# Optimization experiments

Measured on AMD Instinct MI355X. Metric: run time of the kernel, lower is better.

Reference implementation:

```python
import jax, jax.numpy as jnp
import numpy as np

EPS = 1e-5
P, B, T, C = 2, 8, 1024, 1024
H = 4 * C

def layernorm(x, g, b):
    mu = jnp.mean(x, axis=-1, keepdims=True)
    var = jnp.var(x, axis=-1, keepdims=True)
    return (x - mu) * jax.lax.rsqrt(var + EPS) * g + b

def time_shift(x):
    # ZeroPad2d((0,0,1,-1)): xx[t] = x[t-1], xx[0] = 0 along the T axis
    pad = [(0, 0)] * (x.ndim - 2) + [(1, 0), (0, 0)]
    return jnp.pad(x, pad)[..., :-1, :]

def wkv(time_decay, time_first, k, v):
    # Faithful port of the RWKV-v4 CUDA WKV scan (numerically stable form).
    # k, v: [N, T, C]; time_decay/time_first: [C]
    w = -jnp.exp(time_decay)  # decay (negative)
    u = time_first
    kT = jnp.moveaxis(k, 1, 0)  # [T, N, C]
    vT = jnp.moveaxis(v, 1, 0)
    N = k.shape[0]
    Cc = k.shape[2]

    def step(carry, kv):
        aa, bb, pp = carry
        kk, vv = kv
        ww = u + kk
        p = jnp.maximum(pp, ww)
        e1 = jnp.exp(pp - p)
        e2 = jnp.exp(ww - p)
        y = (e1 * aa + e2 * vv) / (e1 * bb + e2)
        ww2 = w + pp
        p2 = jnp.maximum(ww2, kk)
        e1b = jnp.exp(ww2 - p2)
        e2b = jnp.exp(kk - p2)
        return (e1b * aa + e2b * vv, e1b * bb + e2b, p2), y

    init = (jnp.zeros((N, Cc), jnp.float32), jnp.zeros((N, Cc), jnp.float32),
            jnp.full((N, Cc), -1e38, jnp.float32))
    _, yT = jax.lax.scan(step, init, (kT, vT))
    return jnp.moveaxis(yT, 0, 1)  # [N, T, C]


def setup_inputs() -> dict:
    key = jax.random.key(0)
    ks = jax.random.split(key, 20)
    f32 = jnp.float32
    layer_id, n_layer = 1, 12
    ratio_0_to_1 = layer_id / (n_layer - 1)
    ratio_1_to_almost0 = 1.0 - layer_id / n_layer
    xcurve = (np.arange(C, dtype=np.float32) / C).reshape(1, 1, C)
    decay_speed = -5 + 8 * (np.arange(C, dtype=np.float32) / (C - 1)) ** (0.7 + 1.3 * ratio_0_to_1)
    zigzag = (np.array([(i + 1) % 3 - 1 for i in range(C)], dtype=np.float32)) * 0.5
    time_first = np.ones(C, dtype=np.float32) * np.log(0.3) + zigzag
    mk = np.stack([xcurve ** ratio_1_to_almost0 for _ in range(P)], 0)  # [P,1,1,C]
    mv = np.stack([xcurve ** ratio_1_to_almost0 + 0.3 * ratio_0_to_1 for _ in range(P)], 0)
    mr = np.stack([xcurve ** (0.5 * ratio_1_to_almost0) for _ in range(P)], 0)
    s = 0.02
    return {
        'x': jax.random.normal(ks[0], (P, B, T, C), f32),
        'ln1_g': jnp.ones((C,), f32), 'ln1_b': jnp.zeros((C,), f32),
        'ln2_g': jnp.ones((C,), f32), 'ln2_b': jnp.zeros((C,), f32),
        'time_decay': jnp.asarray(decay_speed, f32),
        'time_first': jnp.asarray(time_first, f32),
        'att_mix_k': jnp.asarray(mk, f32), 'att_mix_v': jnp.asarray(mv, f32),
        'att_mix_r': jnp.asarray(mr, f32),
        'Wk': jax.random.normal(ks[1], (C, C), f32) * s,
        'Wv': jax.random.normal(ks[2], (C, C), f32) * s,
        'Wr': jax.random.normal(ks[3], (C, C), f32) * s,
        'Wo': jax.random.normal(ks[4], (C, C), f32) * s,
        'cm_mix_k': jnp.asarray(mk, f32), 'cm_mix_r': jnp.asarray(mk, f32),
        'Wck': jax.random.normal(ks[5], (H, C), f32) * s,
        'Wcr': jax.random.normal(ks[6], (C, C), f32) * s,
        'Wcv': jax.random.normal(ks[7], (C, H), f32) * s,
    }


def reference(x, ln1_g, ln1_b, ln2_g, ln2_b, time_decay, time_first,
              att_mix_k, att_mix_v, att_mix_r, Wk, Wv, Wr, Wo,
              cm_mix_k, cm_mix_r, Wck, Wcr, Wcv):
    p, b, t, c = x.shape
    # --- TimeMix branch: x = x + Wo @ (sigmoid(r) * WKV(k, v)) ---
    h = layernorm(x, ln1_g, ln1_b)
    xx = time_shift(h)
    xk = h * att_mix_k + xx * (1 - att_mix_k)
    xv = h * att_mix_v + xx * (1 - att_mix_v)
    xr = h * att_mix_r + xx * (1 - att_mix_r)
    k = jnp.einsum('pbtc,dc->pbtd', xk, Wk)
    v = jnp.einsum('pbtc,dc->pbtd', xv, Wv)
    sr = jax.nn.sigmoid(jnp.einsum('pbtc,dc->pbtd', xr, Wr))
    y = wkv(time_decay, time_first,
            k.reshape(p * b, t, c), v.reshape(p * b, t, c)).reshape(p, b, t, c)
    x = x + jnp.einsum('pbtc,dc->pbtd', sr * y, Wo)
    # --- ChannelMix branch ---
    h = layernorm(x, ln2_g, ln2_b)
    xx = time_shift(h)
    xk = h * cm_mix_k + xx * (1 - cm_mix_k)
    xr = h * cm_mix_r + xx * (1 - cm_mix_r)
    kk = jnp.einsum('pbtc,hc->pbth', xk, Wck)
    kk = jnp.square(jax.nn.relu(kk))
    kv = jnp.einsum('pbth,ch->pbtc', kk, Wcv)
    out = jax.nn.sigmoid(jnp.einsum('pbtc,dc->pbtd', xr, Wcr)) * kv
    return x + out
```

## Files before the change

kernel.cpp:

```cpp
#include <hip/hip_runtime.h>

#define T_SEQ 1024
#define C_DIM 1024
#define H_DIM 4096
#define M_ROWS 16384
#define CHUNKS 16
#define CLEN 64

typedef _Float16 f16x8 __attribute__((ext_vector_type(8)));
typedef _Float16 f16x4 __attribute__((ext_vector_type(4)));
typedef float    f32x4 __attribute__((ext_vector_type(4)));

#define AS1 __attribute__((address_space(1)))
#define AS3 __attribute__((address_space(3)))

__device__ __forceinline__ void gload_lds16(const void* g, void* l) {
  __builtin_amdgcn_global_load_lds((const AS1 void*)g, (AS3 void*)l, 16, 0, 0);
}

__device__ __forceinline__ float sigmoidf_(float x) {
  return 1.0f / (1.0f + __expf(-x));
}

struct CvtArgs {
  const float* src[7];
  _Float16*    dst[7];
  int n4[7];
  int start[8];
};

__global__ __launch_bounds__(256) void cvt_all_kernel(CvtArgs a) {
  const int bid = blockIdx.x;
  int s = 0;
#pragma unroll
  for (int j = 0; j < 7; ++j) s += (bid >= a.start[j + 1]) ? 1 : 0;
  const int i = (bid - a.start[s]) * 256 + threadIdx.x;
  if (i >= a.n4[s]) return;
  f32x4 v = reinterpret_cast<const f32x4*>(a.src[s])[i];
  f16x4 o;
  o[0] = (_Float16)v[0]; o[1] = (_Float16)v[1];
  o[2] = (_Float16)v[2]; o[3] = (_Float16)v[3];
  reinterpret_cast<f16x4*>(a.dst[s])[i] = o;
}

__global__ __launch_bounds__(256) void ln_kernel(const float* __restrict__ x,
    const float* __restrict__ g, const float* __restrict__ b,
    _Float16* __restrict__ h) {
  const int row  = blockIdx.x * 4 + (threadIdx.x >> 6);
  const int lane = threadIdx.x & 63;
  const f32x4* xr = reinterpret_cast<const f32x4*>(x + (size_t)row * C_DIM);
  f32x4 v[4];
  float s = 0.f, sq = 0.f;
#pragma unroll
  for (int i = 0; i < 4; ++i) {
    v[i] = xr[i * 64 + lane];
#pragma unroll
    for (int j = 0; j < 4; ++j) { s += v[i][j]; sq += v[i][j] * v[i][j]; }
  }
#pragma unroll
  for (int off = 32; off > 0; off >>= 1) {
    s  += __shfl_xor(s, off, 64);
    sq += __shfl_xor(sq, off, 64);
  }
  const float mu   = s * (1.0f / C_DIM);
  const float var  = sq * (1.0f / C_DIM) - mu * mu;
  const float rstd = rsqrtf(var + 1e-5f);
  const f32x4* g4 = reinterpret_cast<const f32x4*>(g);
  const f32x4* b4 = reinterpret_cast<const f32x4*>(b);
  f16x4* h4 = reinterpret_cast<f16x4*>(h + (size_t)row * C_DIM);
#pragma unroll
  for (int i = 0; i < 4; ++i) {
    f32x4 gg = g4[i * 64 + lane];
    f32x4 bb = b4[i * 64 + lane];
    f16x4 o;
#pragma unroll
    for (int j = 0; j < 4; ++j)
      o[j] = (_Float16)((v[i][j] - mu) * rstd * gg[j] + bb[j]);
    h4[i * 64 + lane] = o;
  }
}

__global__ __launch_bounds__(256) void mix3_kernel(const _Float16* __restrict__ h,
    const float* __restrict__ mk, const float* __restrict__ mv, const float* __restrict__ mr,
    _Float16* __restrict__ xk, _Float16* __restrict__ xv, _Float16* __restrict__ xr) {
  const int i  = blockIdx.x * 256 + threadIdx.x;
  const int m  = i >> 7;
  const int c0 = (i & 127) << 3;
  const int p  = m >> 13;
  const int t  = m & (T_SEQ - 1);
  const f16x8* h8 = reinterpret_cast<const f16x8*>(h);
  f16x8 hc = h8[i];
  f16x8 hp;
#pragma unroll
  for (int j = 0; j < 8; ++j) hp[j] = (_Float16)0.f;
  if (t) hp = h8[i - 128];
  f16x8 ok, ov, orr;
#pragma unroll
  for (int j = 0; j < 8; ++j) {
    const float hcf = (float)hc[j], hpf = (float)hp[j];
    const float a = mk[p * C_DIM + c0 + j];
    const float c = mv[p * C_DIM + c0 + j];
    const float d = mr[p * C_DIM + c0 + j];
    ok[j]  = (_Float16)(hcf * a + hpf * (1.f - a));
    ov[j]  = (_Float16)(hcf * c + hpf * (1.f - c));
    orr[j] = (_Float16)(hcf * d + hpf * (1.f - d));
  }
  reinterpret_cast<f16x8*>(xk)[i] = ok;
  reinterpret_cast<f16x8*>(xv)[i] = ov;
  reinterpret_cast<f16x8*>(xr)[i] = orr;
}

__global__ __launch_bounds__(256) void mix2_kernel(const _Float16* __restrict__ h,
    const float* __restrict__ mk, const float* __restrict__ mr,
    _Float16* __restrict__ xk, _Float16* __restrict__ xr) {
  const int i  = blockIdx.x * 256 + threadIdx.x;
  const int m  = i >> 7;
  const int c0 = (i & 127) << 3;
  const int p  = m >> 13;
  const int t  = m & (T_SEQ - 1);
  const f16x8* h8 = reinterpret_cast<const f16x8*>(h);
  f16x8 hc = h8[i];
  f16x8 hp;
#pragma unroll
  for (int j = 0; j < 8; ++j) hp[j] = (_Float16)0.f;
  if (t) hp = h8[i - 128];
  f16x8 ok, orr;
#pragma unroll
  for (int j = 0; j < 8; ++j) {
    const float hcf = (float)hc[j], hpf = (float)hp[j];
    const float a = mk[p * C_DIM + c0 + j];
    const float d = mr[p * C_DIM + c0 + j];
    ok[j]  = (_Float16)(hcf * a + hpf * (1.f - a));
    orr[j] = (_Float16)(hcf * d + hpf * (1.f - d));
  }
  reinterpret_cast<f16x8*>(xk)[i] = ok;
  reinterpret_cast<f16x8*>(xr)[i] = orr;
}

__global__ __launch_bounds__(1024, 1) void wkv_kernel(const _Float16* __restrict__ k,
    const _Float16* __restrict__ v, const _Float16* __restrict__ r,
    const float* __restrict__ td, const float* __restrict__ tf,
    _Float16* __restrict__ a_out) {
  __shared__ float sA[CHUNKS][64];
  __shared__ float sB[CHUNKS][64];
  __shared__ float sP[CHUNKS][64];
  const int tid   = threadIdx.x;
  const int chunk = tid >> 6;
  const int ch    = tid & 63;
  const int n     = blockIdx.x >> 4;
  const int cg    = blockIdx.x & 15;
  const int c     = cg * 64 + ch;
  const float w = -__expf(td[c]);
  const float u = tf[c];
  const size_t cbase = (size_t)n * T_SEQ * C_DIM + (size_t)chunk * CLEN * C_DIM + c;

  float aa = 0.f, bb = 0.f, pp = -1e38f;
  for (int s = 0; s < CLEN; ++s) {
    const size_t idx = cbase + (size_t)s * C_DIM;
    const float kk = (float)k[idx];
    const float vv = (float)v[idx];
    const float ww2 = w + pp;
    const float p2  = fmaxf(ww2, kk);
    const float e1b = __expf(ww2 - p2);
    const float e2b = __expf(kk - p2);
    aa = e1b * aa + e2b * vv;
    bb = e1b * bb + e2b;
    pp = p2;
  }
  sA[chunk][ch] = aa; sB[chunk][ch] = bb; sP[chunk][ch] = pp;
  __syncthreads();

  if (chunk == 0) {
    float pa = 0.f, pb = 0.f, ppr = -1e38f;
    const float wL = w * (float)CLEN;
    for (int j = 0; j < CHUNKS; ++j) {
      const float la = sA[j][ch], lb = sB[j][ch], lp = sP[j][ch];
      sA[j][ch] = pa; sB[j][ch] = pb; sP[j][ch] = ppr;
      const float dp = wL + ppr;
      const float np = fmaxf(dp, lp);
      const float e1 = __expf(dp - np);
      const float e2 = __expf(lp - np);
      pa  = e1 * pa + e2 * la;
      pb  = e1 * pb + e2 * lb;
      ppr = np;
    }
  }
  __syncthreads();

  aa = sA[chunk][ch]; bb = sB[chunk][ch]; pp = sP[chunk][ch];
  for (int s = 0; s < CLEN; ++s) {
    const size_t idx = cbase + (size_t)s * C_DIM;
    const float kk = (float)k[idx];
    const float vv = (float)v[idx];
    const float ww = u + kk;
    const float p  = fmaxf(pp, ww);
    const float e1 = __expf(pp - p);
    const float e2 = __expf(ww - p);
    const float yv = __fdividef(e1 * aa + e2 * vv, e1 * bb + e2);
    const float sr = sigmoidf_((float)r[idx]);
    a_out[idx] = (_Float16)(sr * yv);
    const float ww2 = w + pp;
    const float p2  = fmaxf(ww2, kk);
    const float e1b = __expf(ww2 - p2);
    const float e2b = __expf(kk - p2);
    aa = e1b * aa + e2b * vv;
    bb = e1b * bb + e2b;
    pp = p2;
  }
}

#define GBAR() do { __builtin_amdgcn_sched_barrier(0); \
                    __builtin_amdgcn_s_barrier(); \
                    __builtin_amdgcn_sched_barrier(0); } while (0)
#define WVN(n) do { asm volatile("s_waitcnt vmcnt(" #n ")" ::: "memory"); \
                    __builtin_amdgcn_sched_barrier(0); } while (0)
#define WLN(n) do { asm volatile("s_waitcnt lgkmcnt(" #n ")" ::: "memory"); \
                    __builtin_amdgcn_sched_barrier(0); } while (0)
#define SCHED() __builtin_amdgcn_sched_barrier(0)
#define STAGE(op, SRC, row0, k0, bb) do { \
    _Pragma("unroll") \
    for (int c_ = 0; c_ < 2; ++c_) { \
      gload_lds16((SRC) + (size_t)((row0) + c_ * 64) * K + (k0), \
                  &lds[bb][op][((size_t)((row0) + c_ * 64) << 6) + dbase]); \
    } } while (0)
#define RD_A4(dst, mh, kk_) do { \
    _Pragma("unroll") for (int i_ = 0; i_ < 4; ++i_) \
      dst[i_][kk_] = *reinterpret_cast<const f16x8*>( \
        &lds[bi][0][((wr * 128 + (mh) * 64 + i_ * 16 + frow) << 6) + \
                    ((((kk_) << 5) + fk) ^ fxorh)]); \
  } while (0)
#define RD_B4(kk_) do { \
    _Pragma("unroll") for (int j_ = 0; j_ < 4; ++j_) \
      bf[j_][kk_] = *reinterpret_cast<const f16x8*>( \
        &lds[bi][1][((wcn * 64 + j_ * 16 + frow) << 6) + \
                    ((((kk_) << 5) + fk) ^ fxorh)]); \
  } while (0)
#define MMC(asrc, kk_, half) do { \
    __builtin_amdgcn_s_setprio(1); \
    _Pragma("unroll") for (int i_ = 0; i_ < 4; ++i_) \
    _Pragma("unroll") for (int j_ = 0; j_ < 4; ++j_) \
      acc[(half) * 4 + i_][j_] = __builtin_amdgcn_mfma_f32_16x16x32_f16( \
        asrc[i_][kk_], bf[j_][kk_], acc[(half) * 4 + i_][j_], 0, 0, 0); \
    __builtin_amdgcn_s_setprio(0); \
  } while (0)

template<int EPI>
__global__ __launch_bounds__(512, 2) void gemm_nt_256(
    const _Float16* __restrict__ A, const _Float16* __restrict__ B,
    void* __restrict__ Cv, const float* __restrict__ X,
    const _Float16* __restrict__ KV, int M, int N, int K,
    size_t strideA, size_t strideB, size_t strideCbytes) {
  __shared__ _Float16 lds[2][2][256 * 64];
  const int tid  = threadIdx.x;
  const int wave = tid >> 6;
  const int lane = tid & 63;
  const int wr   = wave >> 2;
  const int wcn  = wave & 3;

  A  = A + (size_t)blockIdx.z * strideA;
  B  = B + (size_t)blockIdx.z * strideB;
  Cv = (void*)((char*)Cv + (size_t)blockIdx.z * strideCbytes);

  const unsigned nwx  = gridDim.x;
  const unsigned pery = gridDim.y >> 3;
  const unsigned id   = blockIdx.y * nwx + blockIdx.x;
  const unsigned xcd  = id & 7;
  const unsigned loc  = id >> 3;
  const size_t m0 = (size_t)(xcd * pery + loc / nwx) * 256;
  const size_t n0 = (size_t)(loc % nwx) * 256;

  const int srow  = tid >> 3;
  const int scolh = ((tid & 7) ^ (srow & 7)) << 3;
  const size_t dbase = (size_t)(srow & ~7) << 6;
  const _Float16* sA = A + (m0 + srow) * (size_t)K + scolh;
  const _Float16* sB = B + (n0 + srow) * (size_t)K + scolh;

  const int frow  = lane & 15;
  const int fk    = (lane >> 4) << 3;
  const int fxorh = (frow & 7) << 3;

  f32x4 acc[8][4];
#pragma unroll
  for (int i = 0; i < 8; ++i)
#pragma unroll
    for (int j = 0; j < 4; ++j) acc[i][j] = (f32x4){0.f, 0.f, 0.f, 0.f};

  STAGE(0, sA, 0, 0, 0); STAGE(0, sA, 128, 0, 0);
  STAGE(1, sB, 0, 0, 0); STAGE(1, sB, 128, 0, 0);

  const int NT = K >> 6;
  for (int t = 0; t < NT; ++t) {
    const int bi = t & 1;
    const int nb = bi ^ 1;
    const int k1 = (t + 1) << 6;
    if (t + 1 < NT) {
      STAGE(0, sA, 0, k1, nb); STAGE(0, sA, 128, k1, nb);
      STAGE(1, sB, 0, k1, nb); STAGE(1, sB, 128, k1, nb);
      WVN(8);
    } else {
      WVN(0);
    }
    GBAR();
    f16x8 a0[4][2], a1[4][2], bf[4][2];
    RD_A4(a0, 0, 0); SCHED();
    RD_B4(0);        SCHED();
    RD_A4(a0, 0, 1); SCHED();
    RD_B4(1);        SCHED();
    WLN(8);
    MMC(a0, 0, 0);
    RD_A4(a1, 1, 0); SCHED();
    WLN(4);
    MMC(a0, 1, 0);
    RD_A4(a1, 1, 1); SCHED();
    WLN(4);
    MMC(a1, 0, 1);
    WLN(0);
    MMC(a1, 1, 1);
    GBAR();
  }

  const int ecol  = lane & 15;
  const int erow4 = (lane >> 4) * 4;
#pragma unroll
  for (int mf = 0; mf < 8; ++mf)
#pragma unroll
    for (int nf = 0; nf < 4; ++nf) {
      const size_t rbase = m0 + (size_t)(wr * 128 + mf * 16 + erow4);
      const size_t cc    = n0 + (size_t)(wcn * 64 + nf * 16 + ecol);
#pragma unroll
      for (int r = 0; r < 4; ++r) {
        const float val = acc[mf][nf][r];
        const size_t off = (rbase + r) * (size_t)N + cc;
        if constexpr (EPI == 0) {
          ((_Float16*)Cv)[off] = (_Float16)val;
        } else if constexpr (EPI == 1) {
          const float tq = fmaxf(val, 0.f);
          ((_Float16*)Cv)[off] = (_Float16)(tq * tq);
        } else if constexpr (EPI == 2) {
          ((float*)Cv)[off] = val + X[off];
        } else {
          ((float*)Cv)[off] = X[off] + sigmoidf_(val) * (float)KV[off];
        }
      }
    }
}

extern "C" void kernel_launch(void* const* d_in, const int* in_sizes, int n_in,
                              void* d_out, int out_size, void* d_ws, size_t ws_size,
                              hipStream_t stream) {
  const float* x      = (const float*)d_in[0];
  const float* ln1_g  = (const float*)d_in[1];
  const float* ln1_b  = (const float*)d_in[2];
  const float* ln2_g  = (const float*)d_in[3];
  const float* ln2_b  = (const float*)d_in[4];
  const float* tdec   = (const float*)d_in[5];
  const float* tfirst = (const float*)d_in[6];
  const float* amk    = (const float*)d_in[7];
  const float* amv    = (const float*)d_in[8];
  const float* amr    = (const float*)d_in[9];
  const float* Wk     = (const float*)d_in[10];
  const float* Wv     = (const float*)d_in[11];
  const float* Wr     = (const float*)d_in[12];
  const float* Wo     = (const float*)d_in[13];
  const float* cmk    = (const float*)d_in[14];
  const float* cmr    = (const float*)d_in[15];
  const float* Wck    = (const float*)d_in[16];
  const float* Wcr    = (const float*)d_in[17];
  const float* Wcv    = (const float*)d_in[18];

  char* ws = (char*)d_ws;
  const size_t SZ = (size_t)M_ROWS * C_DIM * sizeof(_Float16);
  _Float16* B0 = (_Float16*)(ws + 0 * SZ);
  _Float16* B1 = (_Float16*)(ws + 1 * SZ);
  _Float16* B2 = (_Float16*)(ws + 2 * SZ);
  _Float16* B3 = (_Float16*)(ws + 3 * SZ);
  _Float16* B4 = (_Float16*)(ws + 4 * SZ);
  _Float16* B5 = (_Float16*)(ws + 5 * SZ);
  _Float16* B6 = (_Float16*)(ws + 6 * SZ);
  _Float16* wWk  = (_Float16*)(ws + 7 * SZ);
  _Float16* wWv  = wWk  + (size_t)C_DIM * C_DIM;
  _Float16* wWr  = wWv  + (size_t)C_DIM * C_DIM;
  _Float16* wWo  = wWr  + (size_t)C_DIM * C_DIM;
  _Float16* wWcr = wWo  + (size_t)C_DIM * C_DIM;
  _Float16* wWck = wWcr + (size_t)C_DIM * C_DIM;
  _Float16* wWcv = wWck + (size_t)H_DIM * C_DIM;

  {
    CvtArgs a;
    const float* srcs[7] = {Wk, Wv, Wr, Wo, Wcr, Wck, Wcv};
    _Float16*    dsts[7] = {wWk, wWv, wWr, wWo, wWcr, wWck, wWcv};
    const size_t ns[7]   = {(size_t)C_DIM * C_DIM, (size_t)C_DIM * C_DIM,
                            (size_t)C_DIM * C_DIM, (size_t)C_DIM * C_DIM,
                            (size_t)C_DIM * C_DIM, (size_t)H_DIM * C_DIM,
                            (size_t)C_DIM * H_DIM};
    int st = 0;
    for (int j = 0; j < 7; ++j) {
      a.src[j] = srcs[j]; a.dst[j] = dsts[j];
      a.n4[j] = (int)(ns[j] / 4);
      a.start[j] = st;
      st += (a.n4[j] + 255) / 256;
    }
    a.start[7] = st;
    cvt_all_kernel<<<dim3(st), dim3(256), 0, stream>>>(a);
  }

  const dim3 blk(256);
  const dim3 gblk(512);
  const dim3 gN1(C_DIM / 256, M_ROWS / 256);
  const dim3 gKVR(C_DIM / 256, M_ROWS / 256, 3);
  const dim3 gN4(H_DIM / 256, M_ROWS / 256);

  ln_kernel<<<dim3(M_ROWS / 4), blk, 0, stream>>>(x, ln1_g, ln1_b, B0);
  mix3_kernel<<<dim3(M_ROWS * 128 / 256), blk, 0, stream>>>(B0, amk, amv, amr, B1, B2, B3);
  gemm_nt_256<0><<<gKVR, gblk, 0, stream>>>(B1, wWk, B4, nullptr, nullptr,
      M_ROWS, C_DIM, C_DIM,
      (size_t)M_ROWS * C_DIM, (size_t)C_DIM * C_DIM,
      (size_t)M_ROWS * C_DIM * sizeof(_Float16));
  wkv_kernel<<<dim3(256), dim3(1024), 0, stream>>>(B4, B5, B6, tdec, tfirst, B1);
  gemm_nt_256<2><<<gN1, gblk, 0, stream>>>(B1, wWo, d_out, x, nullptr,
      M_ROWS, C_DIM, C_DIM, 0, 0, 0);

  ln_kernel<<<dim3(M_ROWS / 4), blk, 0, stream>>>((const float*)d_out, ln2_g, ln2_b, B0);
  mix2_kernel<<<dim3(M_ROWS * 128 / 256), blk, 0, stream>>>(B0, cmk, cmr, B1, B2);
  gemm_nt_256<1><<<gN4, gblk, 0, stream>>>(B1, wWck, B3, nullptr, nullptr,
      M_ROWS, H_DIM, C_DIM, 0, 0, 0);
  gemm_nt_256<0><<<gN1, gblk, 0, stream>>>(B3, wWcv, B1, nullptr, nullptr,
      M_ROWS, C_DIM, H_DIM, 0, 0, 0);
  gemm_nt_256<3><<<gN1, gblk, 0, stream>>>(B2, wWcr, d_out, (const float*)d_out, B1,
      M_ROWS, C_DIM, C_DIM, 0, 0, 0);
}
```

Measured before the change: 659.5 us.

## Split GEMM K-tile into two half-K LDS segments with staggered staging

Reorganizes the LDS tile layout of the 256x256 fp16 GEMM into two 32-wide K halves with a new XOR swizzle. The main loop now runs two segments per 64-wide K step, each with its own barrier and vmcnt wait, and interleaves the next tile's A and B global-to-LDS loads between the segments. The goal is finer-grained overlap of global loads with MFMA work and fewer LDS bank conflicts. The risks are an extra barrier per K step and a subtle swizzle or wait-count error that could corrupt data.

```diff
diff --git a/kernel.cpp b/kernel.cpp
--- a/kernel.cpp
+++ b/kernel.cpp
@@ -217,31 +217,40 @@
 #define WLN(n) do { asm volatile("s_waitcnt lgkmcnt(" #n ")" ::: "memory"); \
                     __builtin_amdgcn_sched_barrier(0); } while (0)
 #define SCHED() __builtin_amdgcn_sched_barrier(0)
-#define STAGE(op, SRC, row0, k0, bb) do { \
-    _Pragma("unroll") \
-    for (int c_ = 0; c_ < 2; ++c_) { \
-      gload_lds16((SRC) + (size_t)((row0) + c_ * 64) * K + (k0), \
-                  &lds[bb][op][((size_t)((row0) + c_ * 64) << 6) + dbase]); \
-    } } while (0)
-#define RD_A4(dst, mh, kk_) do { \
+#define STAGEU(op, SRCP, kh, k0, bb) do { \
+    gload_lds16((SRCP) + (kh) * 32 + (k0), &lds[bb][op][kh][wave * 16][0]); \
+    gload_lds16((SRCP) + (size_t)128 * K + (kh) * 32 + (k0), \
+                &lds[bb][op][kh][128 + wave * 16][0]); \
+  } while (0)
+#define RD_A4K(dst, mbase, kh) do { \
     _Pragma("unroll") for (int i_ = 0; i_ < 4; ++i_) \
-      dst[i_][kk_] = *reinterpret_cast<const f16x8*>( \
-        &lds[bi][0][((wr * 128 + (mh) * 64 + i_ * 16 + frow) << 6) + \
-                    ((((kk_) << 5) + fk) ^ fxorh)]); \
+      dst[i_] = *reinterpret_cast<const f16x8*>( \
+        &lds[bi][0][kh][wr * 128 + ((mbase) + i_) * 16 + frow][rdoffH]); \
   } while (0)
-#define RD_B4(kk_) do { \
+#define RD_B4K(dst, kh) do { \
     _Pragma("unroll") for (int j_ = 0; j_ < 4; ++j_) \
-      bf[j_][kk_] = *reinterpret_cast<const f16x8*>( \
-        &lds[bi][1][((wcn * 64 + j_ * 16 + frow) << 6) + \
-                    ((((kk_) << 5) + fk) ^ fxorh)]); \
+      dst[j_] = *reinterpret_cast<const f16x8*>( \
+        &lds[bi][1][kh][wcn * 64 + j_ * 16 + frow][rdoffH]); \
   } while (0)
-#define MMC(asrc, kk_, half) do { \
+#define MMC4(asrc, bsrc, rbase) do { \
     __builtin_amdgcn_s_setprio(1); \
     _Pragma("unroll") for (int i_ = 0; i_ < 4; ++i_) \
     _Pragma("unroll") for (int j_ = 0; j_ < 4; ++j_) \
-      acc[(half) * 4 + i_][j_] = __builtin_amdgcn_mfma_f32_16x16x32_f16( \
-        asrc[i_][kk_], bf[j_][kk_], acc[(half) * 4 + i_][j_], 0, 0, 0); \
+      acc[(rbase) + i_][j_] = __builtin_amdgcn_mfma_f32_16x16x32_f16( \
+        asrc[i_], bsrc[j_], acc[(rbase) + i_][j_], 0, 0, 0); \
     __builtin_amdgcn_s_setprio(0); \
+  } while (0)
+#define SEGMENT(KH, WLAST) do { \
+    if (st) { STAGEU(0, sA, KH, k1, nb); WVN(6); } else { WVN(WLAST); } \
+    GBAR(); \
+    f16x8 a0[4], a1[4], b0[4]; \
+    RD_A4K(a0, 0, KH); RD_B4K(b0, KH); SCHED(); \
+    RD_A4K(a1, 4, KH); SCHED(); \
+    if (st) STAGEU(1, sB, KH, k1, nb); \
+    WLN(4); \
+    MMC4(a0, b0, 0); \
+    WLN(0); \
+    MMC4(a1, b0, 4); \
   } while (0)
 
 template<int EPI>
@@ -250,7 +259,7 @@
     void* __restrict__ Cv, const float* __restrict__ X,
     const _Float16* __restrict__ KV, int M, int N, int K,
     size_t strideA, size_t strideB, size_t strideCbytes) {
-  __shared__ _Float16 lds[2][2][256 * 64];
+  __shared__ _Float16 lds[2][2][2][256][32];
   const int tid  = threadIdx.x;
   const int wave = tid >> 6;
   const int lane = tid & 63;
@@ -269,15 +278,13 @@
   const size_t m0 = (size_t)(xcd * pery + loc / nwx) * 256;
   const size_t n0 = (size_t)(loc % nwx) * 256;
 
-  const int srow  = tid >> 3;
-  const int scolh = ((tid & 7) ^ (srow & 7)) << 3;
-  const size_t dbase = (size_t)(srow & ~7) << 6;
-  const _Float16* sA = A + (m0 + srow) * (size_t)K + scolh;
-  const _Float16* sB = B + (n0 + srow) * (size_t)K + scolh;
-
-  const int frow  = lane & 15;
-  const int fk    = (lane >> 4) << 3;
-  const int fxorh = (frow & 7) << 3;
+  const int srowS   = wave * 16 + (lane >> 2);
+  const int srcslot = (lane & 3) ^ (((lane >> 2) ^ (lane >> 4)) & 3);
+  const _Float16* sA = A + (m0 + srowS) * (size_t)K + srcslot * 8;
+  const _Float16* sB = B + (n0 + srowS) * (size_t)K + srcslot * 8;
+
+  const int frow   = lane & 15;
+  const int rdoffH = (((lane >> 4) ^ ((frow ^ (frow >> 2)) & 3)) << 3);
 
   f32x4 acc[8][4];
 #pragma unroll
@@ -285,38 +292,19 @@
 #pragma unroll
     for (int j = 0; j < 4; ++j) acc[i][j] = (f32x4){0.f, 0.f, 0.f, 0.f};
 
-  STAGE(0, sA, 0, 0, 0); STAGE(0, sA, 128, 0, 0);
-  STAGE(1, sB, 0, 0, 0); STAGE(1, sB, 128, 0, 0);
+  STAGEU(0, sA, 0, 0, 0);
+  STAGEU(1, sB, 0, 0, 0);
+  STAGEU(0, sA, 1, 0, 0);
+  STAGEU(1, sB, 1, 0, 0);
 
   const int NT = K >> 6;
   for (int t = 0; t < NT; ++t) {
     const int bi = t & 1;
     const int nb = bi ^ 1;
     const int k1 = (t + 1) << 6;
-    if (t + 1 < NT) {
-      STAGE(0, sA, 0, k1, nb); STAGE(0, sA, 128, k1, nb);
-      STAGE(1, sB, 0, k1, nb); STAGE(1, sB, 128, k1, nb);
-      WVN(8);
-    } else {
-      WVN(0);
-    }
-    GBAR();
-    f16x8 a0[4][2], a1[4][2], bf[4][2];
-    RD_A4(a0, 0, 0); SCHED();
-    RD_B4(0);        SCHED();
-    RD_A4(a0, 0, 1); SCHED();
-    RD_B4(1);        SCHED();
-    WLN(8);
-    MMC(a0, 0, 0);
-    RD_A4(a1, 1, 0); SCHED();
-    WLN(4);
-    MMC(a0, 1, 0);
-    RD_A4(a1, 1, 1); SCHED();
-    WLN(4);
-    MMC(a1, 0, 1);
-    WLN(0);
-    MMC(a1, 1, 1);
-    GBAR();
+    const bool st = (t + 1) < NT;
+    SEGMENT(0, 4);
+    SEGMENT(1, 0);
   }
 
   const int ecol  = lane & 15;
```

New measurement: 654.6 us. No clear change (-0.7%).
